# Kernel tuning notes

Hardware: AMD Instinct MI355X
Metric: run time of the kernel (lower is better)

Reference implementation:

```python
import jax, jax.numpy as jnp
import numpy as np

SUP_NUM = 2048
EPS_NORM = 1e-12
EPS_BN = 1e-5


def l2norm(v, axis):
    n = jnp.sqrt(jnp.sum(v * v, axis=axis, keepdims=True))
    return v / jnp.maximum(n, EPS_NORM)


def segment_mean(vals, ids, num_segments):
    # vals: [N, C], ids: [N] int -> [num_segments, C]
    s = jax.ops.segment_sum(vals, ids, num_segments=num_segments)
    cnt = jax.ops.segment_sum(jnp.ones((vals.shape[0],), vals.dtype), ids, num_segments=num_segments)
    return s / jnp.maximum(cnt, 1.0)[:, None]


def setup_inputs() -> dict:
    key = jax.random.key(0)
    ks = jax.random.split(key, 6)
    B, Cin, H, W = 1, 3, 1024, 1024
    Cf = 32
    x = jax.random.normal(ks[0], (B, Cin, H, W), dtype=jnp.float32)
    conv_feat = jax.random.normal(ks[1], (B, Cf, H, W), dtype=jnp.float32)
    vit_feature = jax.random.normal(ks[2], (B, SUP_NUM, Cf), dtype=jnp.float32)
    seg_ids = jax.random.randint(ks[3], (B * H * W,), 0, SUP_NUM, dtype=jnp.int32)
    w_soft = jax.random.normal(ks[4], (1, 2 * Cf, 3), dtype=jnp.float32) * 0.1
    b_soft = jnp.zeros((1,), jnp.float32)
    bn_gamma = jnp.ones((1,), jnp.float32)
    bn_beta = jnp.zeros((1,), jnp.float32)
    return {"x": x, "conv_feat": conv_feat, "vit_feature": vit_feature, "seg_ids": seg_ids,
            "w_soft": w_soft, "b_soft": b_soft, "bn_gamma": bn_gamma, "bn_beta": bn_beta}


def reference(x, conv_feat, vit_feature, seg_ids, w_soft, b_soft, bn_gamma, bn_beta):
    B, Cf, H, W = conv_feat.shape
    Cin = x.shape[1]
    # F.normalize(conv, p=2, dim=1)
    conv_1 = l2norm(conv_feat, axis=1)
    # [B,C,H,W] -> [B*H*W, C]
    F1 = conv_1.transpose(0, 2, 3, 1).reshape(-1, Cf)
    X = jax.lax.stop_gradient(x).transpose(0, 2, 3, 1).reshape(-1, Cin)
    # superpixel scatter-mean (replaces the per-segment Python loop)
    M_F = segment_mean(F1, seg_ids, SUP_NUM)                  # [Sup, Cf]
    X_F = segment_mean(X, seg_ids, SUP_NUM)                   # [Sup, Cin]
    M_F = M_F.reshape(B, SUP_NUM, Cf)
    X_F = X_F.reshape(B, SUP_NUM, Cin).transpose(0, 2, 1)     # [B, Cin, Sup]
    vit_n = l2norm(vit_feature, axis=-1)
    all_F = jnp.concatenate([M_F, vit_n], axis=-1).transpose(0, 2, 1)  # [B, 2Cf, Sup]
    all_F = l2norm(all_F, axis=1)
    # Conv1d(2Cf -> 1, k=3, pad=1)
    z = jax.lax.conv_general_dilated(all_F, w_soft, window_strides=(1,), padding=((1, 1),),
                                     dimension_numbers=("NCH", "OIH", "NCH")) + b_soft[None, :, None]
    # BatchNorm1d (training-mode batch stats over (B, L))
    mu = jnp.mean(z, axis=(0, 2), keepdims=True)
    var = jnp.mean((z - mu) ** 2, axis=(0, 2), keepdims=True)
    z = bn_gamma[None, :, None] * (z - mu) / jnp.sqrt(var + EPS_BN) + bn_beta[None, :, None]
    result = jax.nn.sigmoid(z)                                # [B, 1, Sup]
    gap = jnp.mean(result, axis=-1, keepdims=True)            # AdaptiveAvgPool1d(1)
    return (result, gap, all_F, X_F)
```

## Files before the change

### kernel.cpp

```cpp
#include <hip/hip_runtime.h>
#include <hip/hip_bf16.h>
#include <hip/hip_fp16.h>

#define SUP 2048
#define NB  256

#define SC_CONV 1024.0f
#define SC_X0   512.0f
#define SC_XLO  256.0f
#define ISC_CONV (1.0f/1024.0f)
#define ISC_X0   (1.0f/512.0f)
#define ISC_XLO  (1.0f/256.0f)

__device__ __forceinline__ int enc2i(int qa, int qb) {
    return ((qa - (qb < 0 ? 1 : 0)) << 16) + (qb & 0xFFFF);
}
__device__ __forceinline__ int enc2f(float a, float b) {
    return enc2i(__float2int_rn(a), __float2int_rn(b));
}

__global__ __launch_bounds__(1024) void k_segfused(const float* __restrict__ conv,
                                                   const float* __restrict__ x,
                                                   const int* __restrict__ ids,
                                                   float* __restrict__ accum,
                                                   __half* __restrict__ pbuf,
                                                   int npix) {
    __shared__ int sacc[18 * SUP];
    for (int i = threadIdx.x; i < 18 * SUP; i += blockDim.x) sacc[i] = 0;
    __syncthreads();

    int per = ((npix + (int)gridDim.x - 1) / (int)gridDim.x + 1) & ~1;
    int start = blockIdx.x * per;
    int end = min(start + per, npix);
    int stride2 = (int)blockDim.x * 2;

    int p = start + (int)threadIdx.x * 2;
    for (; p + 1 < end; p += stride2) {
        int2 id2 = *(const int2*)(ids + p);
        float2 cv[32];
        float s0 = 0.f, s1 = 0.f;
#pragma unroll
        for (int c = 0; c < 32; ++c) {
            cv[c] = *(const float2*)(conv + (size_t)c * npix + p);
            s0 += cv[c].x * cv[c].x;
            s1 += cv[c].y * cv[c].y;
        }
        float i0 = 1.0f / fmaxf(sqrtf(s0), 1e-12f);
        float i1 = 1.0f / fmaxf(sqrtf(s1), 1e-12f);
#pragma unroll
        for (int r = 0; r < 16; ++r) {
            float2 a = cv[2 * r], b = cv[2 * r + 1];
            atomicAdd(&sacc[r * SUP + id2.x],
                      enc2f(a.x * i0 * SC_CONV, b.x * i0 * SC_CONV));
            atomicAdd(&sacc[r * SUP + id2.y],
                      enc2f(a.y * i1 * SC_CONV, b.y * i1 * SC_CONV));
        }
        float2 x0 = *(const float2*)(x + p);
        float2 x1 = *(const float2*)(x + (size_t)npix + p);
        float2 x2 = *(const float2*)(x + (size_t)2 * npix + p);
        atomicAdd(&sacc[16 * SUP + id2.x], enc2f(x0.x * SC_X0, x1.x * SC_XLO));
        atomicAdd(&sacc[16 * SUP + id2.y], enc2f(x0.y * SC_X0, x1.y * SC_XLO));
        atomicAdd(&sacc[17 * SUP + id2.x], enc2i(1, __float2int_rn(x2.x * SC_XLO)));
        atomicAdd(&sacc[17 * SUP + id2.y], enc2i(1, __float2int_rn(x2.y * SC_XLO)));
    }
    if (p == end - 1) {
        int s = ids[p];
        float cvv[32];
        float ss = 0.f;
#pragma unroll
        for (int c = 0; c < 32; ++c) {
            cvv[c] = conv[(size_t)c * npix + p];
            ss += cvv[c] * cvv[c];
        }
        float iv = 1.0f / fmaxf(sqrtf(ss), 1e-12f);
#pragma unroll
        for (int r = 0; r < 16; ++r)
            atomicAdd(&sacc[r * SUP + s],
                      enc2f(cvv[2 * r] * iv * SC_CONV, cvv[2 * r + 1] * iv * SC_CONV));
        atomicAdd(&sacc[16 * SUP + s],
                  enc2f(x[p] * SC_X0, x[(size_t)npix + p] * SC_XLO));
        atomicAdd(&sacc[17 * SUP + s],
                  enc2i(1, __float2int_rn(x[(size_t)2 * npix + p] * SC_XLO)));
    }
    __syncthreads();

    for (int i = threadIdx.x; i < 18 * SUP; i += blockDim.x) {
        int S = sacc[i];
        int qb = (int)(short)(S & 0xFFFF);
        int qa = (S - qb) >> 16;
        int row = i >> 11;
        int s = i & (SUP - 1);
        int hi_row, lo_row;
        float fhi, flo;
        if (row < 16) {
            hi_row = 2 * row; lo_row = 2 * row + 1;
            fhi = (float)qa * ISC_CONV;
            flo = (float)qb * ISC_CONV;
        } else if (row == 16) {
            hi_row = 32; lo_row = 33;
            fhi = (float)qa * ISC_X0;
            flo = (float)qb * ISC_XLO;
        } else {
            hi_row = 35; lo_row = 34;
            fhi = (float)qa;
            flo = (float)qb * ISC_XLO;
        }
        if (pbuf) {
            __half* dst = pbuf + (size_t)blockIdx.x * 36 * SUP;
            dst[hi_row * SUP + s] = __float2half(fhi);
            dst[lo_row * SUP + s] = __float2half(flo);
        } else {
            unsafeAtomicAdd(&accum[hi_row * SUP + s], fhi);
            unsafeAtomicAdd(&accum[lo_row * SUP + s], flo);
        }
    }
}

__global__ __launch_bounds__(64) void k_reduce(const __half* __restrict__ pbuf,
                                               float* __restrict__ accum) {
    int j8 = (blockIdx.x * 64 + threadIdx.x) * 8;
    if (j8 >= 36 * SUP) return;
    float s[8];
#pragma unroll
    for (int k = 0; k < 8; ++k) s[k] = 0.f;
    for (int b = 0; b < NB; ++b) {
        uint4 u = *(const uint4*)(pbuf + (size_t)b * 36 * SUP + j8);
        __half2 h0 = *reinterpret_cast<__half2*>(&u.x);
        __half2 h1 = *reinterpret_cast<__half2*>(&u.y);
        __half2 h2 = *reinterpret_cast<__half2*>(&u.z);
        __half2 h3 = *reinterpret_cast<__half2*>(&u.w);
        float2 f0 = __half22float2(h0), f1 = __half22float2(h1);
        float2 f2 = __half22float2(h2), f3 = __half22float2(h3);
        s[0] += f0.x; s[1] += f0.y; s[2] += f1.x; s[3] += f1.y;
        s[4] += f2.x; s[5] += f2.y; s[6] += f3.x; s[7] += f3.y;
    }
    float4 o0 = {s[0], s[1], s[2], s[3]};
    float4 o1 = {s[4], s[5], s[6], s[7]};
    *(float4*)(accum + j8) = o0;
    *(float4*)(accum + j8 + 4) = o1;
}

__device__ __forceinline__ void compute_col(const float* __restrict__ accum,
                                            const float* __restrict__ vit,
                                            int g, float* __restrict__ col) {
    if (g < 0 || g >= SUP) {
#pragma unroll
        for (int c = 0; c < 64; ++c) col[c] = 0.f;
        return;
    }
    float cnt = fmaxf(accum[35 * SUP + g], 1.0f);
    float rc = 1.0f / cnt;
#pragma unroll
    for (int c = 0; c < 32; ++c) col[c] = accum[c * SUP + g] * rc;
    float vs = 0.f;
#pragma unroll
    for (int c = 0; c < 32; ++c) {
        float v = vit[g * 32 + c];
        col[32 + c] = v;
        vs += v * v;
    }
    float vinv = 1.0f / fmaxf(sqrtf(vs), 1e-12f);
#pragma unroll
    for (int c = 0; c < 32; ++c) col[32 + c] *= vinv;
    float ssq = 0.f;
#pragma unroll
    for (int c = 0; c < 64; ++c) ssq += col[c] * col[c];
    float ainv = 1.0f / fmaxf(sqrtf(ssq), 1e-12f);
#pragma unroll
    for (int c = 0; c < 64; ++c) col[c] *= ainv;
}

__global__ __launch_bounds__(256) void k_finalconv(const float* __restrict__ accum,
                                                   const float* __restrict__ vit,
                                                   const float* __restrict__ w,
                                                   const float* __restrict__ bias,
                                                   float* __restrict__ allF_out,
                                                   float* __restrict__ xf_out,
                                                   float* __restrict__ z_out) {
    __shared__ float L[258][65];
    __shared__ float sw[192];
    int t = threadIdx.x;
    int b0 = blockIdx.x * 256;
    if (t < 192) sw[t] = w[t];

    float col[64];
    int g = b0 + t;
    compute_col(accum, vit, g, col);
#pragma unroll
    for (int c = 0; c < 64; ++c) L[t + 1][c] = col[c];
#pragma unroll
    for (int c = 0; c < 64; ++c) allF_out[c * SUP + g] = col[c];
    {
        float cnt = fmaxf(accum[35 * SUP + g], 1.0f);
        float rc = 1.0f / cnt;
#pragma unroll
        for (int c = 0; c < 3; ++c)
            xf_out[c * SUP + g] = accum[(32 + c) * SUP + g] * rc;
    }
    if (t == 0) {
        compute_col(accum, vit, b0 - 1, col);
#pragma unroll
        for (int c = 0; c < 64; ++c) L[0][c] = col[c];
    }
    if (t == 255) {
        compute_col(accum, vit, b0 + 256, col);
#pragma unroll
        for (int c = 0; c < 64; ++c) L[257][c] = col[c];
    }
    __syncthreads();

    float acc = bias[0];
#pragma unroll
    for (int c = 0; c < 64; ++c) {
        acc += sw[c * 3] * L[t][c] + sw[c * 3 + 1] * L[t + 1][c]
             + sw[c * 3 + 2] * L[t + 2][c];
    }
    z_out[b0 + t] = acc;
}

__global__ __launch_bounds__(512) void k_head2(const float* __restrict__ z,
                                               const float* __restrict__ gamma,
                                               const float* __restrict__ beta,
                                               float* __restrict__ out) {
    __shared__ float red[8];
    __shared__ float bc[2];
    int tid = threadIdx.x;
    int lane = tid & 63, wid = tid >> 6;

    float zs[4];
#pragma unroll
    for (int j = 0; j < 4; ++j) zs[j] = z[j * 512 + tid];

    float s1 = zs[0] + zs[1] + zs[2] + zs[3];
#pragma unroll
    for (int o = 32; o > 0; o >>= 1) s1 += __shfl_down(s1, o);
    if (lane == 0) red[wid] = s1;
    __syncthreads();
    if (tid == 0) {
        float t = 0.f;
        for (int i = 0; i < 8; ++i) t += red[i];
        bc[0] = t / (float)SUP;
    }
    __syncthreads();
    float mu = bc[0];

    float s2 = 0.f;
#pragma unroll
    for (int j = 0; j < 4; ++j) { float d = zs[j] - mu; s2 += d * d; }
#pragma unroll
    for (int o = 32; o > 0; o >>= 1) s2 += __shfl_down(s2, o);
    __syncthreads();
    if (lane == 0) red[wid] = s2;
    __syncthreads();
    if (tid == 0) {
        float t = 0.f;
        for (int i = 0; i < 8; ++i) t += red[i];
        bc[1] = t / (float)SUP;
    }
    __syncthreads();
    float var = bc[1];

    float invstd = rsqrtf(var + 1e-5f);
    float gm = gamma[0], bt = beta[0];
    float gsum = 0.f;
#pragma unroll
    for (int j = 0; j < 4; ++j) {
        int p = j * 512 + tid;
        float zn = gm * (zs[j] - mu) * invstd + bt;
        float r = 1.0f / (1.0f + expf(-zn));
        out[p] = r;
        gsum += r;
    }
#pragma unroll
    for (int o = 32; o > 0; o >>= 1) gsum += __shfl_down(gsum, o);
    __syncthreads();
    if (lane == 0) red[wid] = gsum;
    __syncthreads();
    if (tid == 0) {
        float t = 0.f;
        for (int i = 0; i < 8; ++i) t += red[i];
        out[SUP] = t / (float)SUP;
    }
}

extern "C" void kernel_launch(void* const* d_in, const int* in_sizes, int n_in,
                              void* d_out, int out_size, void* d_ws, size_t ws_size,
                              hipStream_t stream) {
    const float* x     = (const float*)d_in[0];
    const float* conv  = (const float*)d_in[1];
    const float* vit   = (const float*)d_in[2];
    const int*   ids   = (const int*)d_in[3];
    const float* w     = (const float*)d_in[4];
    const float* b     = (const float*)d_in[5];
    const float* gamma = (const float*)d_in[6];
    const float* beta  = (const float*)d_in[7];
    float* out = (float*)d_out;

    int npix = in_sizes[3];

    float* accum = (float*)d_ws;
    float* zbuf = accum + 36 * SUP;
    __half* pbuf = (__half*)(zbuf + SUP);

    size_t need = (36 * SUP + SUP) * sizeof(float)
                + (size_t)NB * 36 * SUP * sizeof(__half);
    bool useP = ws_size >= need;

    if (!useP) hipMemsetAsync(accum, 0, 36 * SUP * sizeof(float), stream);

    k_segfused<<<NB, 1024, 0, stream>>>(conv, x, ids, accum,
                                        useP ? pbuf : (__half*)nullptr, npix);
    if (useP) {
        k_reduce<<<(36 * SUP / 8 + 63) / 64, 64, 0, stream>>>(pbuf, accum);
    }

    float* allF = out + SUP + 1;
    float* xf = allF + 64 * SUP;
    k_finalconv<<<SUP / 256, 256, 0, stream>>>(accum, vit, w, b, allF, xf, zbuf);

    k_head2<<<1, 512, 0, stream>>>(zbuf, gamma, beta, out);
}
```

Measured before the change: 75.65 us.

## Split segment accumulators between LDS and global 64-bit atomics

Shrinks the per-block shared-memory accumulator from 18 to 12 packed rows. The last 8 normalized conv channels and the 3 input channels plus the count now go to 64-bit packed atomics in a global buffer, which gives them wider fixed-point range. The per-block fp16 partial buffer drops from 36 to 24 rows, and the reduce kernel decodes the global rows directly. The intent is to cut LDS footprint and partial-buffer traffic. The cost is millions of contended global atomics onto only 12K addresses, plus an extra memset.

Measured after the change: 300.7 us. 297% more time.

```diff
diff --git a/kernel.cpp b/kernel.cpp
--- a/kernel.cpp
+++ b/kernel.cpp
@@ -4,13 +4,12 @@
 
 #define SUP 2048
 #define NB  256
+#define LROWS 12
 
 #define SC_CONV 1024.0f
 #define SC_X0   512.0f
 #define SC_XLO  256.0f
 #define ISC_CONV (1.0f/1024.0f)
-#define ISC_X0   (1.0f/512.0f)
-#define ISC_XLO  (1.0f/256.0f)
 
 __device__ __forceinline__ int enc2i(int qa, int qb) {
     return ((qa - (qb < 0 ? 1 : 0)) << 16) + (qb & 0xFFFF);
@@ -18,15 +17,21 @@
 __device__ __forceinline__ int enc2f(float a, float b) {
     return enc2i(__float2int_rn(a), __float2int_rn(b));
 }
+__device__ __forceinline__ unsigned long long enc64(int qa, int qb) {
+    unsigned int hi = (unsigned int)(qa - (qb < 0 ? 1 : 0));
+    return ((unsigned long long)hi << 32) | (unsigned int)qb;
+}
+__device__ __forceinline__ int qrn(float v) { return __float2int_rn(v); }
 
 __global__ __launch_bounds__(1024) void k_segfused(const float* __restrict__ conv,
                                                    const float* __restrict__ x,
                                                    const int* __restrict__ ids,
                                                    float* __restrict__ accum,
+                                                   unsigned long long* __restrict__ gacc,
                                                    __half* __restrict__ pbuf,
                                                    int npix) {
-    __shared__ int sacc[18 * SUP];
-    for (int i = threadIdx.x; i < 18 * SUP; i += blockDim.x) sacc[i] = 0;
+    __shared__ int sacc[LROWS * SUP];
+    for (int i = threadIdx.x; i < LROWS * SUP; i += blockDim.x) sacc[i] = 0;
     __syncthreads();
 
     int per = ((npix + (int)gridDim.x - 1) / (int)gridDim.x + 1) & ~1;
@@ -45,23 +50,29 @@
             s0 += cv[c].x * cv[c].x;
             s1 += cv[c].y * cv[c].y;
         }
-        float i0 = 1.0f / fmaxf(sqrtf(s0), 1e-12f);
-        float i1 = 1.0f / fmaxf(sqrtf(s1), 1e-12f);
-#pragma unroll
-        for (int r = 0; r < 16; ++r) {
+        float w0 = SC_CONV / fmaxf(sqrtf(s0), 1e-12f);
+        float w1 = SC_CONV / fmaxf(sqrtf(s1), 1e-12f);
+#pragma unroll
+        for (int r = 0; r < LROWS; ++r) {
             float2 a = cv[2 * r], b = cv[2 * r + 1];
-            atomicAdd(&sacc[r * SUP + id2.x],
-                      enc2f(a.x * i0 * SC_CONV, b.x * i0 * SC_CONV));
-            atomicAdd(&sacc[r * SUP + id2.y],
-                      enc2f(a.y * i1 * SC_CONV, b.y * i1 * SC_CONV));
+            atomicAdd(&sacc[r * SUP + id2.x], enc2f(a.x * w0, b.x * w0));
+            atomicAdd(&sacc[r * SUP + id2.y], enc2f(a.y * w1, b.y * w1));
+        }
+#pragma unroll
+        for (int k = 0; k < 4; ++k) {
+            float2 a = cv[24 + 2 * k], b = cv[25 + 2 * k];
+            atomicAdd(&gacc[k * SUP + id2.x], enc64(qrn(a.x * w0), qrn(b.x * w0)));
+            atomicAdd(&gacc[k * SUP + id2.y], enc64(qrn(a.y * w1), qrn(b.y * w1)));
         }
         float2 x0 = *(const float2*)(x + p);
         float2 x1 = *(const float2*)(x + (size_t)npix + p);
         float2 x2 = *(const float2*)(x + (size_t)2 * npix + p);
-        atomicAdd(&sacc[16 * SUP + id2.x], enc2f(x0.x * SC_X0, x1.x * SC_XLO));
-        atomicAdd(&sacc[16 * SUP + id2.y], enc2f(x0.y * SC_X0, x1.y * SC_XLO));
-        atomicAdd(&sacc[17 * SUP + id2.x], enc2i(1, __float2int_rn(x2.x * SC_XLO)));
-        atomicAdd(&sacc[17 * SUP + id2.y], enc2i(1, __float2int_rn(x2.y * SC_XLO)));
+        atomicAdd(&gacc[4 * SUP + id2.x],
+                  enc64(qrn(x0.x * SC_CONV), qrn(x1.x * SC_CONV)));
+        atomicAdd(&gacc[4 * SUP + id2.y],
+                  enc64(qrn(x0.y * SC_CONV), qrn(x1.y * SC_CONV)));
+        atomicAdd(&gacc[5 * SUP + id2.x], enc64(1, qrn(x2.x * SC_CONV)));
+        atomicAdd(&gacc[5 * SUP + id2.y], enc64(1, qrn(x2.y * SC_CONV)));
     }
     if (p == end - 1) {
         int s = ids[p];
@@ -72,72 +83,87 @@
             cvv[c] = conv[(size_t)c * npix + p];
             ss += cvv[c] * cvv[c];
         }
-        float iv = 1.0f / fmaxf(sqrtf(ss), 1e-12f);
-#pragma unroll
-        for (int r = 0; r < 16; ++r)
-            atomicAdd(&sacc[r * SUP + s],
-                      enc2f(cvv[2 * r] * iv * SC_CONV, cvv[2 * r + 1] * iv * SC_CONV));
-        atomicAdd(&sacc[16 * SUP + s],
-                  enc2f(x[p] * SC_X0, x[(size_t)npix + p] * SC_XLO));
-        atomicAdd(&sacc[17 * SUP + s],
-                  enc2i(1, __float2int_rn(x[(size_t)2 * npix + p] * SC_XLO)));
-    }
-    __syncthreads();
-
-    for (int i = threadIdx.x; i < 18 * SUP; i += blockDim.x) {
+        float w = SC_CONV / fmaxf(sqrtf(ss), 1e-12f);
+#pragma unroll
+        for (int r = 0; r < LROWS; ++r)
+            atomicAdd(&sacc[r * SUP + s], enc2f(cvv[2 * r] * w, cvv[2 * r + 1] * w));
+#pragma unroll
+        for (int k = 0; k < 4; ++k)
+            atomicAdd(&gacc[k * SUP + s],
+                      enc64(qrn(cvv[24 + 2 * k] * w), qrn(cvv[25 + 2 * k] * w)));
+        atomicAdd(&gacc[4 * SUP + s],
+                  enc64(qrn(x[p] * SC_CONV), qrn(x[(size_t)npix + p] * SC_CONV)));
+        atomicAdd(&gacc[5 * SUP + s],
+                  enc64(1, qrn(x[(size_t)2 * npix + p] * SC_CONV)));
+    }
+    __syncthreads();
+
+    for (int i = threadIdx.x; i < LROWS * SUP; i += blockDim.x) {
         int S = sacc[i];
         int qb = (int)(short)(S & 0xFFFF);
         int qa = (S - qb) >> 16;
         int row = i >> 11;
         int s = i & (SUP - 1);
-        int hi_row, lo_row;
-        float fhi, flo;
-        if (row < 16) {
-            hi_row = 2 * row; lo_row = 2 * row + 1;
-            fhi = (float)qa * ISC_CONV;
-            flo = (float)qb * ISC_CONV;
-        } else if (row == 16) {
-            hi_row = 32; lo_row = 33;
-            fhi = (float)qa * ISC_X0;
-            flo = (float)qb * ISC_XLO;
+        float fhi = (float)qa * ISC_CONV;
+        float flo = (float)qb * ISC_CONV;
+        if (pbuf) {
+            __half* dst = pbuf + (size_t)blockIdx.x * 24 * SUP;
+            dst[(2 * row) * SUP + s] = __float2half(fhi);
+            dst[(2 * row + 1) * SUP + s] = __float2half(flo);
         } else {
-            hi_row = 35; lo_row = 34;
-            fhi = (float)qa;
-            flo = (float)qb * ISC_XLO;
-        }
-        if (pbuf) {
-            __half* dst = pbuf + (size_t)blockIdx.x * 36 * SUP;
-            dst[hi_row * SUP + s] = __float2half(fhi);
-            dst[lo_row * SUP + s] = __float2half(flo);
-        } else {
-            unsafeAtomicAdd(&accum[hi_row * SUP + s], fhi);
-            unsafeAtomicAdd(&accum[lo_row * SUP + s], flo);
+            unsafeAtomicAdd(&accum[(2 * row) * SUP + s], fhi);
+            unsafeAtomicAdd(&accum[(2 * row + 1) * SUP + s], flo);
         }
     }
 }
 
 __global__ __launch_bounds__(64) void k_reduce(const __half* __restrict__ pbuf,
+                                               const unsigned long long* __restrict__ gacc,
                                                float* __restrict__ accum) {
     int j8 = (blockIdx.x * 64 + threadIdx.x) * 8;
     if (j8 >= 36 * SUP) return;
-    float s[8];
-#pragma unroll
-    for (int k = 0; k < 8; ++k) s[k] = 0.f;
-    for (int b = 0; b < NB; ++b) {
-        uint4 u = *(const uint4*)(pbuf + (size_t)b * 36 * SUP + j8);
-        __half2 h0 = *reinterpret_cast<__half2*>(&u.x);
-        __half2 h1 = *reinterpret_cast<__half2*>(&u.y);
-        __half2 h2 = *reinterpret_cast<__half2*>(&u.z);
-        __half2 h3 = *reinterpret_cast<__half2*>(&u.w);
-        float2 f0 = __half22float2(h0), f1 = __half22float2(h1);
-        float2 f2 = __half22float2(h2), f3 = __half22float2(h3);
-        s[0] += f0.x; s[1] += f0.y; s[2] += f1.x; s[3] += f1.y;
-        s[4] += f2.x; s[5] += f2.y; s[6] += f3.x; s[7] += f3.y;
-    }
-    float4 o0 = {s[0], s[1], s[2], s[3]};
-    float4 o1 = {s[4], s[5], s[6], s[7]};
-    *(float4*)(accum + j8) = o0;
-    *(float4*)(accum + j8 + 4) = o1;
+    int row = j8 >> 11;
+    if (row < 24) {
+        float s[8];
+#pragma unroll
+        for (int k = 0; k < 8; ++k) s[k] = 0.f;
+        for (int b = 0; b < NB; ++b) {
+            uint4 u = *(const uint4*)(pbuf + (size_t)b * 24 * SUP + j8);
+            __half2 h0 = *reinterpret_cast<__half2*>(&u.x);
+            __half2 h1 = *reinterpret_cast<__half2*>(&u.y);
+            __half2 h2 = *reinterpret_cast<__half2*>(&u.z);
+            __half2 h3 = *reinterpret_cast<__half2*>(&u.w);
+            float2 f0 = __half22float2(h0), f1 = __half22float2(h1);
+            float2 f2 = __half22float2(h2), f3 = __half22float2(h3);
+            s[0] += f0.x; s[1] += f0.y; s[2] += f1.x; s[3] += f1.y;
+            s[4] += f2.x; s[5] += f2.y; s[6] += f3.x; s[7] += f3.y;
+        }
+        float4 o0 = {s[0], s[1], s[2], s[3]};
+        float4 o1 = {s[4], s[5], s[6], s[7]};
+        *(float4*)(accum + j8) = o0;
+        *(float4*)(accum + j8 + 4) = o1;
+    } else {
+        int sbase = j8 & (SUP - 1);
+#pragma unroll
+        for (int k = 0; k < 8; ++k) {
+            int s = sbase + k;
+            unsigned long long S;
+            bool useHi;
+            float scale = ISC_CONV;
+            if (row < 32) {
+                int slot = (row - 24) >> 1;
+                S = gacc[slot * SUP + s];
+                useHi = (((row - 24) & 1) == 0);
+            } else if (row == 32) { S = gacc[4 * SUP + s]; useHi = true; }
+            else if (row == 33)   { S = gacc[4 * SUP + s]; useHi = false; }
+            else if (row == 34)   { S = gacc[5 * SUP + s]; useHi = false; }
+            else                  { S = gacc[5 * SUP + s]; useHi = true; scale = 1.0f; }
+            int lo = (int)(unsigned int)(S & 0xFFFFFFFFull);
+            long long hi = ((long long)S - (long long)lo) >> 32;
+            float val = (useHi ? (float)hi : (float)lo) * scale;
+            accum[j8 + k] = val;
+        }
+    }
 }
 
 __device__ __forceinline__ void compute_col(const float* __restrict__ accum,
@@ -300,18 +326,22 @@
 
     float* accum = (float*)d_ws;
     float* zbuf = accum + 36 * SUP;
-    __half* pbuf = (__half*)(zbuf + SUP);
-
-    size_t need = (36 * SUP + SUP) * sizeof(float)
-                + (size_t)NB * 36 * SUP * sizeof(__half);
+    unsigned long long* gacc = (unsigned long long*)(zbuf + SUP);
+    __half* pbuf = (__half*)(gacc + 6 * SUP);
+
+    size_t need = (36 * SUP + SUP) * sizeof(float) + 6 * SUP * 8
+                + (size_t)NB * 24 * SUP * sizeof(__half);
     bool useP = ws_size >= need;
 
+    hipMemsetAsync(gacc, 0, 6 * SUP * sizeof(unsigned long long), stream);
     if (!useP) hipMemsetAsync(accum, 0, 36 * SUP * sizeof(float), stream);
 
-    k_segfused<<<NB, 1024, 0, stream>>>(conv, x, ids, accum,
+    k_segfused<<<NB, 1024, 0, stream>>>(conv, x, ids, accum, gacc,
                                         useP ? pbuf : (__half*)nullptr, npix);
     if (useP) {
-        k_reduce<<<(36 * SUP / 8 + 63) / 64, 64, 0, stream>>>(pbuf, accum);
+        k_reduce<<<(36 * SUP / 8 + 63) / 64, 64, 0, stream>>>(pbuf, gacc, accum);
+    } else {
+        k_reduce<<<(36 * SUP / 8 + 63) / 64, 64, 0, stream>>>((const __half*)nullptr, gacc, accum);
     }
 
     float* allF = out + SUP + 1;
```
